# Performance work log

Measured on AMD Instinct MI355X. Metric: run time of the kernel, lower is better.

Reference implementation:

```python
import jax, jax.numpy as jnp
import numpy as np

B, N, FIN, FOUT = 8, 2048, 128, 128


def setup_inputs() -> dict:
    key = jax.random.key(0)
    k1, k2, k3, k4, k5 = jax.random.split(key, 5)
    x = jax.random.normal(k1, (B, N, FIN), dtype=jnp.float32)
    adj = jax.random.randint(k2, (N, N), 0, 2, dtype=jnp.int32)
    # W stored [in, out] (transpose of torch Linear weight; same math via x @ W)
    W = jax.random.normal(k3, (FIN, FOUT), dtype=jnp.float32) * (1.0 / np.sqrt(FIN))
    # a: Linear(2*out, 1) split into src/dst halves: a([h_i,h_j]) = h_i@a_src + h_j@a_dst
    a_src = jax.random.normal(k4, (FOUT,), dtype=jnp.float32) * 0.1
    a_dst = jax.random.normal(k5, (FOUT,), dtype=jnp.float32) * 0.1
    return {"x": x, "adj": adj, "W": W, "a_src": a_src, "a_dst": a_dst}


def reference(x, adj, W, a_src, a_dst):
    # h: [B, N, FOUT]
    h = jnp.einsum('bnf,fo->bno', x, W)
    # attention logits e_ij = LeakyReLU(a_src.h_i + a_dst.h_j), built by broadcast
    s_i = jnp.einsum('bno,o->bn', h, a_src)  # [B, N]
    s_j = jnp.einsum('bno,o->bn', h, a_dst)  # [B, N]
    e = jax.nn.leaky_relu(s_i[:, :, None] + s_j[:, None, :], negative_slope=0.2)  # [B,N,N]
    scores = jnp.where(adj[None, :, :] == 0, -jnp.inf, e)
    attn = jax.nn.softmax(scores, axis=-1)
    attn = jnp.nan_to_num(attn, nan=0.0)  # rows with no neighbors -> all zeros
    # dropout is identity in eval mode
    out = jnp.einsum('bij,bjo->bio', attn, h)  # [B, N, FOUT]
    return out
```

## Files before the change

kernel.cpp:

```cpp
#include <hip/hip_runtime.h>
#include <math.h>

#define BATCH 8
#define NN 2048
#define FF 128

typedef __attribute__((ext_vector_type(4))) float f32x4;
typedef _Float16 half8 __attribute__((ext_vector_type(8)));

__device__ __forceinline__ unsigned short h2u(_Float16 h) {
    return __builtin_bit_cast(unsigned short, h);
}

__global__ __launch_bounds__(256) void k_h(const float* __restrict__ x,
                                           const int* __restrict__ adj,
                                           const float* __restrict__ W,
                                           const float* __restrict__ a_src,
                                           const float* __restrict__ a_dst,
                                           unsigned short* __restrict__ hF,
                                           float* __restrict__ Eg,  float* __restrict__ E2g,
                                           float* __restrict__ Sg,  float* __restrict__ S2g,
                                           unsigned* __restrict__ amT) {
    __shared__ float sred[4 * 16];
    __shared__ float dred[4 * 16];

    const int t = threadIdx.x;
    const int w = t >> 6, lane = t & 63;
    const int nl = lane & 15, quad = lane >> 4;
    const int row0 = blockIdx.x * 16;
    const int b = row0 >> 11, jloc0 = row0 & 2047;
    const int gr = row0 + nl;
    const int nt0 = w * 2;

    {
        const int prow = blockIdx.x * 2 + (w >> 1);
        const int* __restrict__ ar = adj + (size_t)prow * NN;
        const int s0 = (w & 1) * 16;
        #pragma unroll
        for (int s = 0; s < 16; ++s) {
            const int seg = s0 + s;
            const unsigned long long m = __ballot(ar[seg * 64 + lane] != 0);
            if (lane == 0)  amT[(size_t)(seg * 2) * NN + prow] = (unsigned)m;
            if (lane == 32) amT[(size_t)(seg * 2 + 1) * NN + prow] = (unsigned)(m >> 32);
        }
    }

    f32x4 acc[2] = {{0.f,0.f,0.f,0.f},{0.f,0.f,0.f,0.f}};

    #pragma unroll
    for (int ks = 0; ks < 4; ++ks) {
        const float4 xa = *reinterpret_cast<const float4*>(&x[(size_t)gr * FF + ks * 32 + quad * 8]);
        const float4 xb = *reinterpret_cast<const float4*>(&x[(size_t)gr * FF + ks * 32 + quad * 8 + 4]);
        const float xv[8] = {xa.x, xa.y, xa.z, xa.w, xb.x, xb.y, xb.z, xb.w};
        half8 ah, al;
        #pragma unroll
        for (int i = 0; i < 8; ++i) {
            const _Float16 hh = (_Float16)xv[i];
            ah[i] = hh;
            al[i] = (_Float16)(xv[i] - (float)hh);
        }
        #pragma unroll
        for (int nn = 0; nn < 2; ++nn) {
            const float* __restrict__ wp = W + (size_t)(ks * 32 + quad * 8) * FF + (nt0 + nn) * 16 + nl;
            half8 bh, bl;
            #pragma unroll
            for (int j = 0; j < 8; ++j) {
                const float wv = wp[j * FF];
                const _Float16 hh = (_Float16)wv;
                bh[j] = hh;
                bl[j] = (_Float16)(wv - (float)hh);
            }
            acc[nn] = __builtin_amdgcn_mfma_f32_16x16x32_f16(ah, bh, acc[nn], 0, 0, 0);
            acc[nn] = __builtin_amdgcn_mfma_f32_16x16x32_f16(al, bh, acc[nn], 0, 0, 0);
            acc[nn] = __builtin_amdgcn_mfma_f32_16x16x32_f16(ah, bl, acc[nn], 0, 0, 0);
        }
    }

    const int jloc = jloc0 + quad * 4;
    const int jg = jloc >> 3, u0 = jloc & 7;
    #pragma unroll
    for (int nn = 0; nn < 2; ++nn) {
        ushort4 hv;
        hv.x = h2u((_Float16)acc[nn][0]);
        hv.y = h2u((_Float16)acc[nn][1]);
        hv.z = h2u((_Float16)acc[nn][2]);
        hv.w = h2u((_Float16)acc[nn][3]);
        *reinterpret_cast<ushort4*>(&hF[(size_t)b * 262144 + (nt0 + nn) * 32768 + jg * 128 + nl * 8 + u0]) = hv;
    }

    float as[2], ad[2];
    #pragma unroll
    for (int nn = 0; nn < 2; ++nn) {
        const int col = (nt0 + nn) * 16 + nl;
        as[nn] = a_src[col];
        ad[nn] = a_dst[col];
    }
    #pragma unroll
    for (int r = 0; r < 4; ++r) {
        float sp = acc[0][r] * as[0] + acc[1][r] * as[1];
        float dp = acc[0][r] * ad[0] + acc[1][r] * ad[1];
        #pragma unroll
        for (int off = 8; off >= 1; off >>= 1) {
            sp += __shfl_xor(sp, off, 16);
            dp += __shfl_xor(dp, off, 16);
        }
        if (nl == 0) {
            sred[w * 16 + quad * 4 + r] = sp;
            dred[w * 16 + quad * 4 + r] = dp;
        }
    }
    __syncthreads();
    if (t < 16) {
        const float sp = sred[t] + sred[16 + t] + sred[32 + t] + sred[48 + t];
        const float dp = dred[t] + dred[16 + t] + dred[32 + t] + dred[48 + t];
        const int row = row0 + t;
        Sg[row]  = __expf(sp - 2.f);
        S2g[row] = __expf(0.2f * sp - 2.f);
        Eg[row]  = __expf(dp - 2.f);
        E2g[row] = __expf(0.2f * dp - 2.f);
    }
}

__global__ __launch_bounds__(512, 4) void k_attn(const unsigned short* __restrict__ hF,
                                                 const unsigned* __restrict__ amT,
                                                 const float* __restrict__ Eg,
                                                 const float* __restrict__ E2g,
                                                 const float* __restrict__ Sg,
                                                 const float* __restrict__ S2g,
                                                 float* __restrict__ P,
                                                 float* __restrict__ L) {
    __shared__ unsigned short pA[2 * 64 * 72];

    const int t = threadIdx.x;
    const int b = blockIdx.y;
    const int i0 = blockIdx.x * 64;
    const int jh = blockIdx.z;
    const int jbase = jh * 1024;

    const int rp = t >> 4, jw4 = t & 15;
    const int ra = rp * 2, rb = ra + 1;
    const float Sa  = Sg[(size_t)b * NN + i0 + ra];
    const float S2a = S2g[(size_t)b * NN + i0 + ra];
    const float Sb  = Sg[(size_t)b * NN + i0 + rb];
    const float S2b = S2g[(size_t)b * NN + i0 + rb];
    const int bitb = (jw4 & 7) * 4;
    const int pwo = ra * 72 + jw4 * 4;
    const float* __restrict__ Egb  = Eg  + (size_t)b * NN + jbase;
    const float* __restrict__ E2gb = E2g + (size_t)b * NN + jbase;
    const unsigned* __restrict__ amb = amT + (size_t)(jh * 32) * NN + i0;

    const int w = t >> 6, lane = t & 63;
    const int nl = lane & 15, quad = lane >> 4;
    const int mtp = w & 1, ntp = w >> 1;
    const unsigned short* __restrict__ hFb = hF + (size_t)b * 262144;
    int bofs[2], aofs[2];
    #pragma unroll
    for (int nn = 0; nn < 2; ++nn) bofs[nn] = (ntp + nn * 4) * 32768 + (jbase + quad * 8) * 16 + nl * 8;
    #pragma unroll
    for (int mm = 0; mm < 2; ++mm) aofs[mm] = ((mtp + mm * 2) * 16 + nl) * 72 + quad * 8;

    f32x4 acc[2][2] = {{{0.f,0.f,0.f,0.f},{0.f,0.f,0.f,0.f}},{{0.f,0.f,0.f,0.f},{0.f,0.f,0.f,0.f}}};
    float la = 0.f, lb = 0.f;

    for (int tt = 0; tt < 16; ++tt) {
        const int buf = tt & 1;
        const int jofs = tt * 1024;

        half8 bfr[2][2];
        #pragma unroll
        for (int nn = 0; nn < 2; ++nn) {
            bfr[nn][0] = *reinterpret_cast<const half8*>(hFb + bofs[nn] + jofs);
            bfr[nn][1] = *reinterpret_cast<const half8*>(hFb + bofs[nn] + jofs + 512);
        }

        {
            const int jb = tt * 64 + jw4 * 4;
            const float4 ej4  = *reinterpret_cast<const float4*>(&Egb[jb]);
            const float4 e2j4 = *reinterpret_cast<const float4*>(&E2gb[jb]);
            const uint2 mw = *reinterpret_cast<const uint2*>(&amb[(size_t)(tt * 2 + (jw4 >> 3)) * NN + ra]);
            const float ejA[4]  = {ej4.x, ej4.y, ej4.z, ej4.w};
            const float e2jA[4] = {e2j4.x, e2j4.y, e2j4.z, e2j4.w};
            ushort4 ha, hb;
            #pragma unroll
            for (int jj = 0; jj < 4; ++jj) {
                const float ua = fmaxf(Sa * ejA[jj], S2a * e2jA[jj]);
                const float ub = fmaxf(Sb * ejA[jj], S2b * e2jA[jj]);
                const float pa = ((mw.x >> (bitb + jj)) & 1u) ? ua : 0.f;
                const float pb = ((mw.y >> (bitb + jj)) & 1u) ? ub : 0.f;
                la += pa;
                lb += pb;
                ((unsigned short*)&ha)[jj] = h2u((_Float16)pa);
                ((unsigned short*)&hb)[jj] = h2u((_Float16)pb);
            }
            *reinterpret_cast<ushort4*>(&pA[buf * 4608 + pwo]) = ha;
            *reinterpret_cast<ushort4*>(&pA[buf * 4608 + pwo + 72]) = hb;
        }

        __syncthreads();

        half8 afr[2][2];
        #pragma unroll
        for (int mm = 0; mm < 2; ++mm) {
            afr[mm][0] = *reinterpret_cast<const half8*>(&pA[buf * 4608 + aofs[mm]]);
            afr[mm][1] = *reinterpret_cast<const half8*>(&pA[buf * 4608 + aofs[mm] + 32]);
        }
        #pragma unroll
        for (int mm = 0; mm < 2; ++mm) {
            #pragma unroll
            for (int kh = 0; kh < 2; ++kh) {
                acc[mm][0] = __builtin_amdgcn_mfma_f32_16x16x32_f16(afr[mm][kh], bfr[0][kh], acc[mm][0], 0, 0, 0);
                acc[mm][1] = __builtin_amdgcn_mfma_f32_16x16x32_f16(afr[mm][kh], bfr[1][kh], acc[mm][1], 0, 0, 0);
            }
        }
    }

    #pragma unroll
    for (int off = 8; off >= 1; off >>= 1) {
        la += __shfl_xor(la, off, 16);
        lb += __shfl_xor(lb, off, 16);
    }

    float* __restrict__ Pb = P + ((size_t)jh * BATCH + b) * 262144;
    float* __restrict__ Lb = L + ((size_t)jh * BATCH + b) * 2048;
    if (jw4 == 0) {
        Lb[i0 + ra] = la;
        Lb[i0 + rb] = lb;
    }
    #pragma unroll
    for (int mm = 0; mm < 2; ++mm) {
        const int lrow = (mtp + mm * 2) * 16 + quad * 4;
        #pragma unroll
        for (int r = 0; r < 4; ++r) {
            #pragma unroll
            for (int nn = 0; nn < 2; ++nn) {
                const int col = (ntp + nn * 4) * 16 + nl;
                Pb[(size_t)(i0 + lrow + r) * FF + col] = acc[mm][nn][r];
            }
        }
    }
}

__global__ __launch_bounds__(256) void k_comb(const float* __restrict__ P,
                                              const float* __restrict__ L,
                                              float* __restrict__ out) {
    const int g0 = blockIdx.x * 512 + threadIdx.x;
    #pragma unroll
    for (int it = 0; it < 2; ++it) {
        const int g = g0 + it * 256;
        const size_t flat = (size_t)g * 4;
        const int row = (int)(flat >> 7);
        const float l = L[row] + L[16384 + row];
        const float inv = (l > 0.f) ? 1.f / l : 0.f;
        const float4 p0 = *reinterpret_cast<const float4*>(&P[flat]);
        const float4 p1 = *reinterpret_cast<const float4*>(&P[2097152 + flat]);
        *reinterpret_cast<float4*>(&out[flat]) =
            make_float4((p0.x + p1.x) * inv, (p0.y + p1.y) * inv,
                        (p0.z + p1.z) * inv, (p0.w + p1.w) * inv);
    }
}

extern "C" void kernel_launch(void* const* d_in, const int* in_sizes, int n_in,
                              void* d_out, int out_size, void* d_ws, size_t ws_size,
                              hipStream_t stream) {
    const float* x     = (const float*)d_in[0];
    const int*   adj   = (const int*)d_in[1];
    const float* W     = (const float*)d_in[2];
    const float* a_src = (const float*)d_in[3];
    const float* a_dst = (const float*)d_in[4];
    float* out = (float*)d_out;

    unsigned short* hF = (unsigned short*)d_ws;
    float* Eg  = (float*)(hF + 2097152);
    float* E2g = Eg + 16384;
    float* Sg  = E2g + 16384;
    float* S2g = Sg + 16384;
    unsigned* amT = (unsigned*)(S2g + 16384);
    float* P = (float*)(amT + 131072);
    float* L = P + 4194304;

    k_h<<<1024, 256, 0, stream>>>(x, adj, W, a_src, a_dst, hF, Eg, E2g, Sg, S2g, amT);
    k_attn<<<dim3(32, BATCH, 2), 512, 0, stream>>>(hF, amT, Eg, E2g, Sg, S2g, P, L);
    k_comb<<<1024, 256, 0, stream>>>(P, L, out);
}
```

Measured before the change: 113.0 us.

## Drop split-K over neighbors and fuse normalization into attention kernel

The attention kernel no longer splits the neighbor dimension into two halves that write partial P and L buffers for a separate combine kernel. Each block now covers 32 rows over all 2048 neighbors with 1024 threads, reduces the row sums in shared memory and writes the normalized output directly. This removes the combine launch and the round trip of partial results through global memory. In exchange each thread does less per-tile work with a single MFMA accumulator over twice as many tiles, and the grid stays at 512 blocks with larger blocks.

```diff
diff --git a/kernel.cpp b/kernel.cpp
--- a/kernel.cpp
+++ b/kernel.cpp
@@ -121,141 +121,82 @@
     }
 }
 
-__global__ __launch_bounds__(512, 4) void k_attn(const unsigned short* __restrict__ hF,
-                                                 const unsigned* __restrict__ amT,
-                                                 const float* __restrict__ Eg,
-                                                 const float* __restrict__ E2g,
-                                                 const float* __restrict__ Sg,
-                                                 const float* __restrict__ S2g,
-                                                 float* __restrict__ P,
-                                                 float* __restrict__ L) {
-    __shared__ unsigned short pA[2 * 64 * 72];
+__global__ __launch_bounds__(1024, 4) void k_attn(const unsigned short* __restrict__ hF,
+                                                  const unsigned* __restrict__ amT,
+                                                  const float* __restrict__ Eg,
+                                                  const float* __restrict__ E2g,
+                                                  const float* __restrict__ Sg,
+                                                  const float* __restrict__ S2g,
+                                                  float* __restrict__ out) {
+    __shared__ unsigned short pA[2 * 32 * 72];
+    __shared__ float l_s[32];
 
     const int t = threadIdx.x;
     const int b = blockIdx.y;
-    const int i0 = blockIdx.x * 64;
-    const int jh = blockIdx.z;
-    const int jbase = jh * 1024;
-
-    const int rp = t >> 4, jw4 = t & 15;
-    const int ra = rp * 2, rb = ra + 1;
-    const float Sa  = Sg[(size_t)b * NN + i0 + ra];
-    const float S2a = S2g[(size_t)b * NN + i0 + ra];
-    const float Sb  = Sg[(size_t)b * NN + i0 + rb];
-    const float S2b = S2g[(size_t)b * NN + i0 + rb];
-    const int bitb = (jw4 & 7) * 4;
-    const int pwo = ra * 72 + jw4 * 4;
-    const float* __restrict__ Egb  = Eg  + (size_t)b * NN + jbase;
-    const float* __restrict__ E2gb = E2g + (size_t)b * NN + jbase;
-    const unsigned* __restrict__ amb = amT + (size_t)(jh * 32) * NN + i0;
+    const int i0 = blockIdx.x * 32;
+
+    const int prow = t >> 5;
+    const int jp = t & 31;
+    const float Sa  = Sg[(size_t)b * NN + i0 + prow];
+    const float S2a = S2g[(size_t)b * NN + i0 + prow];
+    const int pwo = prow * 72 + jp * 2;
+    const int bit = (jp & 15) * 2;
+    const float* __restrict__ Egb  = Eg  + (size_t)b * NN;
+    const float* __restrict__ E2gb = E2g + (size_t)b * NN;
+    const unsigned* __restrict__ amb = amT + i0 + prow;
 
     const int w = t >> 6, lane = t & 63;
     const int nl = lane & 15, quad = lane >> 4;
-    const int mtp = w & 1, ntp = w >> 1;
+    const int mt = w & 1, nt = w >> 1;
     const unsigned short* __restrict__ hFb = hF + (size_t)b * 262144;
-    int bofs[2], aofs[2];
-    #pragma unroll
-    for (int nn = 0; nn < 2; ++nn) bofs[nn] = (ntp + nn * 4) * 32768 + (jbase + quad * 8) * 16 + nl * 8;
-    #pragma unroll
-    for (int mm = 0; mm < 2; ++mm) aofs[mm] = ((mtp + mm * 2) * 16 + nl) * 72 + quad * 8;
-
-    f32x4 acc[2][2] = {{{0.f,0.f,0.f,0.f},{0.f,0.f,0.f,0.f}},{{0.f,0.f,0.f,0.f},{0.f,0.f,0.f,0.f}}};
-    float la = 0.f, lb = 0.f;
-
-    for (int tt = 0; tt < 16; ++tt) {
+    const int bofs = nt * 32768 + quad * 128 + nl * 8;
+    const int aofs = (mt * 16 + nl) * 72 + quad * 8;
+
+    f32x4 acc = {0.f, 0.f, 0.f, 0.f};
+    float la = 0.f;
+
+    for (int tt = 0; tt < 32; ++tt) {
         const int buf = tt & 1;
         const int jofs = tt * 1024;
 
-        half8 bfr[2][2];
-        #pragma unroll
-        for (int nn = 0; nn < 2; ++nn) {
-            bfr[nn][0] = *reinterpret_cast<const half8*>(hFb + bofs[nn] + jofs);
-            bfr[nn][1] = *reinterpret_cast<const half8*>(hFb + bofs[nn] + jofs + 512);
-        }
+        const half8 b0 = *reinterpret_cast<const half8*>(hFb + bofs + jofs);
+        const half8 b1 = *reinterpret_cast<const half8*>(hFb + bofs + jofs + 512);
 
         {
-            const int jb = tt * 64 + jw4 * 4;
-            const float4 ej4  = *reinterpret_cast<const float4*>(&Egb[jb]);
-            const float4 e2j4 = *reinterpret_cast<const float4*>(&E2gb[jb]);
-            const uint2 mw = *reinterpret_cast<const uint2*>(&amb[(size_t)(tt * 2 + (jw4 >> 3)) * NN + ra]);
-            const float ejA[4]  = {ej4.x, ej4.y, ej4.z, ej4.w};
-            const float e2jA[4] = {e2j4.x, e2j4.y, e2j4.z, e2j4.w};
-            ushort4 ha, hb;
-            #pragma unroll
-            for (int jj = 0; jj < 4; ++jj) {
-                const float ua = fmaxf(Sa * ejA[jj], S2a * e2jA[jj]);
-                const float ub = fmaxf(Sb * ejA[jj], S2b * e2jA[jj]);
-                const float pa = ((mw.x >> (bitb + jj)) & 1u) ? ua : 0.f;
-                const float pb = ((mw.y >> (bitb + jj)) & 1u) ? ub : 0.f;
-                la += pa;
-                lb += pb;
-                ((unsigned short*)&ha)[jj] = h2u((_Float16)pa);
-                ((unsigned short*)&hb)[jj] = h2u((_Float16)pb);
-            }
-            *reinterpret_cast<ushort4*>(&pA[buf * 4608 + pwo]) = ha;
-            *reinterpret_cast<ushort4*>(&pA[buf * 4608 + pwo + 72]) = hb;
+            const int jb = tt * 64 + jp * 2;
+            const float2 ej  = *reinterpret_cast<const float2*>(&Egb[jb]);
+            const float2 e2j = *reinterpret_cast<const float2*>(&E2gb[jb]);
+            const unsigned mw = amb[(size_t)(tt * 2 + (jp >> 4)) * NN];
+            const float u0 = fmaxf(Sa * ej.x, S2a * e2j.x);
+            const float u1 = fmaxf(Sa * ej.y, S2a * e2j.y);
+            const float p0 = ((mw >> bit) & 1u) ? u0 : 0.f;
+            const float p1 = ((mw >> (bit + 1)) & 1u) ? u1 : 0.f;
+            la += p0 + p1;
+            const unsigned pk = (unsigned)h2u((_Float16)p0) |
+                                ((unsigned)h2u((_Float16)p1) << 16);
+            *reinterpret_cast<unsigned*>(&pA[buf * 2304 + pwo]) = pk;
         }
 
         __syncthreads();
 
-        half8 afr[2][2];
-        #pragma unroll
-        for (int mm = 0; mm < 2; ++mm) {
-            afr[mm][0] = *reinterpret_cast<const half8*>(&pA[buf * 4608 + aofs[mm]]);
-            afr[mm][1] = *reinterpret_cast<const half8*>(&pA[buf * 4608 + aofs[mm] + 32]);
-        }
-        #pragma unroll
-        for (int mm = 0; mm < 2; ++mm) {
-            #pragma unroll
-            for (int kh = 0; kh < 2; ++kh) {
-                acc[mm][0] = __builtin_amdgcn_mfma_f32_16x16x32_f16(afr[mm][kh], bfr[0][kh], acc[mm][0], 0, 0, 0);
-                acc[mm][1] = __builtin_amdgcn_mfma_f32_16x16x32_f16(afr[mm][kh], bfr[1][kh], acc[mm][1], 0, 0, 0);
-            }
-        }
-    }
-
-    #pragma unroll
-    for (int off = 8; off >= 1; off >>= 1) {
-        la += __shfl_xor(la, off, 16);
-        lb += __shfl_xor(lb, off, 16);
-    }
-
-    float* __restrict__ Pb = P + ((size_t)jh * BATCH + b) * 262144;
-    float* __restrict__ Lb = L + ((size_t)jh * BATCH + b) * 2048;
-    if (jw4 == 0) {
-        Lb[i0 + ra] = la;
-        Lb[i0 + rb] = lb;
-    }
-    #pragma unroll
-    for (int mm = 0; mm < 2; ++mm) {
-        const int lrow = (mtp + mm * 2) * 16 + quad * 4;
-        #pragma unroll
-        for (int r = 0; r < 4; ++r) {
-            #pragma unroll
-            for (int nn = 0; nn < 2; ++nn) {
-                const int col = (ntp + nn * 4) * 16 + nl;
-                Pb[(size_t)(i0 + lrow + r) * FF + col] = acc[mm][nn][r];
-            }
-        }
-    }
-}
-
-__global__ __launch_bounds__(256) void k_comb(const float* __restrict__ P,
-                                              const float* __restrict__ L,
-                                              float* __restrict__ out) {
-    const int g0 = blockIdx.x * 512 + threadIdx.x;
-    #pragma unroll
-    for (int it = 0; it < 2; ++it) {
-        const int g = g0 + it * 256;
-        const size_t flat = (size_t)g * 4;
-        const int row = (int)(flat >> 7);
-        const float l = L[row] + L[16384 + row];
+        const half8 a0 = *reinterpret_cast<const half8*>(&pA[buf * 2304 + aofs]);
+        const half8 a1 = *reinterpret_cast<const half8*>(&pA[buf * 2304 + aofs + 32]);
+        acc = __builtin_amdgcn_mfma_f32_16x16x32_f16(a0, b0, acc, 0, 0, 0);
+        acc = __builtin_amdgcn_mfma_f32_16x16x32_f16(a1, b1, acc, 0, 0, 0);
+    }
+
+    #pragma unroll
+    for (int off = 16; off >= 1; off >>= 1) la += __shfl_xor(la, off, 32);
+    if (jp == 0) l_s[prow] = la;
+    __syncthreads();
+
+    const int col = nt * 16 + nl;
+    #pragma unroll
+    for (int r = 0; r < 4; ++r) {
+        const int lrow = mt * 16 + quad * 4 + r;
+        const float l = l_s[lrow];
         const float inv = (l > 0.f) ? 1.f / l : 0.f;
-        const float4 p0 = *reinterpret_cast<const float4*>(&P[flat]);
-        const float4 p1 = *reinterpret_cast<const float4*>(&P[2097152 + flat]);
-        *reinterpret_cast<float4*>(&out[flat]) =
-            make_float4((p0.x + p1.x) * inv, (p0.y + p1.y) * inv,
-                        (p0.z + p1.z) * inv, (p0.w + p1.w) * inv);
+        out[((size_t)b * NN + i0 + lrow) * FF + col] = acc[r] * inv;
     }
 }
 
@@ -275,10 +216,7 @@
     float* Sg  = E2g + 16384;
     float* S2g = Sg + 16384;
     unsigned* amT = (unsigned*)(S2g + 16384);
-    float* P = (float*)(amT + 131072);
-    float* L = P + 4194304;
 
     k_h<<<1024, 256, 0, stream>>>(x, adj, W, a_src, a_dst, hF, Eg, E2g, Sg, S2g, amT);
-    k_attn<<<dim3(32, BATCH, 2), 512, 0, stream>>>(hF, amT, Eg, E2g, Sg, S2g, P, L);
-    k_comb<<<1024, 256, 0, stream>>>(P, L, out);
-}
+    k_attn<<<dim3(NN / 32, BATCH), 1024, 0, stream>>>(hF, amT, Eg, E2g, Sg, S2g, out);
+}
```

After: 131.6 us. 16.4% more time.
